# Kernel optimization log

Measured on AMD Instinct MI355X. Metric: run time of the kernel, lower is better.

Reference implementation:

```python
import jax, jax.numpy as jnp
import numpy as np

B = 4096
P = 10000          # points per cloud (hard-coded view(-1,3,10000))
NUM_POINTS = 100   # forced by phi.view(-1, 300)
BOX_SIZE = 0.5
H_G = 128
H_L = 128


def setup_inputs() -> dict:
    key = jax.random.key(0)
    ks = jax.random.split(key, 12)
    x = jax.random.uniform(ks[0], (B, 3, P, 1), dtype=jnp.float32)
    l_t_prev = jax.random.uniform(ks[1], (B, 3), dtype=jnp.float32)
    sc = 0.02
    W1 = jax.random.normal(ks[2], (H_G, NUM_POINTS * 3), dtype=jnp.float32) * sc
    b1 = jnp.zeros((H_G,), jnp.float32)
    W2 = jax.random.normal(ks[3], (H_L, 3), dtype=jnp.float32) * sc
    b2 = jnp.zeros((H_L,), jnp.float32)
    W3 = jax.random.normal(ks[4], (H_G + H_L, H_G), dtype=jnp.float32) * sc
    b3 = jnp.zeros((H_G + H_L,), jnp.float32)
    W4 = jax.random.normal(ks[5], (H_G + H_L, H_L), dtype=jnp.float32) * sc
    b4 = jnp.zeros((H_G + H_L,), jnp.float32)
    return {"x": x, "l_t_prev": l_t_prev, "W1": W1, "b1": b1, "W2": W2,
            "b2": b2, "W3": W3, "b3": b3, "W4": W4, "b4": b4}


def _foveate(x, l):
    # x: (B,3,P,1) -> pts: (B,3,P)
    pts = x.reshape(x.shape[0], 3, P)
    half = BOX_SIZE / 2.0
    lo = l - half  # (B,3)
    hi = l + half
    # per-point in-box mask over all 3 axes: (B,P)
    inside = jnp.all((pts >= lo[:, :, None]) & (pts <= hi[:, :, None]), axis=1)
    count = inside.sum(axis=-1)  # (B,)
    # stable argsort puts in-box point indices first, preserving order
    order = jnp.argsort(~inside, axis=-1, stable=True)  # (B,P)
    pos = jnp.arange(NUM_POINTS)
    # deterministic stand-in for random subsample/pad: take first NUM_POINTS
    # in-box points, wrapping (repeating) if fewer than NUM_POINTS exist
    safe = pos[None, :] % jnp.maximum(count, 1)[:, None]  # (B,NUM_POINTS)
    idx = jnp.take_along_axis(order, safe, axis=-1)  # (B,NUM_POINTS)
    idx3 = jnp.broadcast_to(idx[:, None, :], (pts.shape[0], 3, NUM_POINTS))
    sel = jnp.take_along_axis(pts, idx3, axis=2)  # (B,3,NUM_POINTS)
    # empty boxes -> zero fill (matches torch.zeros fill_box branch)
    sel = jnp.where(count[:, None, None] > 0, sel, jnp.zeros_like(sel))
    return sel.reshape(pts.shape[0], 3 * NUM_POINTS)  # (B,300)


def reference(x, l_t_prev, W1, b1, W2, b2, W3, b3, W4, b4):
    phi = _foveate(x, l_t_prev)                       # (B,300)
    phi_out = jax.nn.relu(phi @ W1.T + b1)            # (B,h_g)
    l_out = jax.nn.relu(l_t_prev @ W2.T + b2)         # (B,h_l)
    what = phi_out @ W3.T + b3                        # (B,h_g+h_l)
    where = l_out @ W4.T + b4                         # (B,h_g+h_l)
    return jax.nn.relu(what + where)
```

## Files before the change

### kernel.cpp

```cpp
#include <hip/hip_runtime.h>

#define P_PTS 10000
#define NPTS 100
#define TB 8

__global__ __launch_bounds__(256) void foveate_kernel(
    const float* __restrict__ x,
    const float* __restrict__ l,
    float* __restrict__ phi)
{
    const int b   = blockIdx.x;
    const int tid = threadIdx.x;
    const int wid = tid >> 6, lane = tid & 63;

    __shared__ float s_phi[3][NPTS];
    __shared__ int s_wcnt[4];

    const float lx = l[b * 3 + 0];
    const float ly = l[b * 3 + 1];
    const float lz = l[b * 3 + 2];
    const float lox = lx - 0.25f, hix = lx + 0.25f;
    const float loy = ly - 0.25f, hiy = ly + 0.25f;
    const float loz = lz - 0.25f, hiz = lz + 0.25f;

    const float* xb = x + (size_t)b * 3 * P_PTS;

    int cnt = 0;
    for (int base = 0; base < P_PTS; base += 256) {
        const int p = base + tid;
        bool inside = false;
        float x0 = 0.f, x1 = 0.f, x2 = 0.f;
        if (p < P_PTS) {
            x0 = xb[p];
            x1 = xb[P_PTS + p];
            x2 = xb[2 * P_PTS + p];
            inside = (x0 >= lox) && (x0 <= hix) &&
                     (x1 >= loy) && (x1 <= hiy) &&
                     (x2 >= loz) && (x2 <= hiz);
        }
        const unsigned long long m = __ballot(inside);
        if (lane == 0) s_wcnt[wid] = __popcll(m);
        __syncthreads();
        int prefix = 0, total = 0;
        #pragma unroll
        for (int w = 0; w < 4; ++w) {
            const int c = s_wcnt[w];
            total += c;
            if (w < wid) prefix += c;
        }
        const int mypos = cnt + prefix +
                          __popcll(m & ((1ull << lane) - 1ull));
        if (inside && mypos < NPTS) {
            s_phi[0][mypos] = x0;
            s_phi[1][mypos] = x1;
            s_phi[2][mypos] = x2;
        }
        cnt += total;
        __syncthreads();
        if (cnt >= NPTS) break;
    }

    const int n = (cnt < NPTS) ? cnt : NPTS;
    if (n == 0) {
        for (int j = tid; j < 3 * NPTS; j += 256)
            ((float*)s_phi)[j] = 0.0f;
    } else if (n < NPTS) {
        for (int j = n + tid; j < NPTS; j += 256) {
            const int src = j % n;
            s_phi[0][j] = s_phi[0][src];
            s_phi[1][j] = s_phi[1][src];
            s_phi[2][j] = s_phi[2][src];
        }
    }
    __syncthreads();

    for (int j = tid; j < 3 * NPTS; j += 256)
        phi[(size_t)b * 300 + j] = ((const float*)s_phi)[j];
}

__global__ __launch_bounds__(256) void mlp_kernel(
    const float* __restrict__ phi,
    const float* __restrict__ l,
    const float* __restrict__ W1,
    const float* __restrict__ b1,
    const float* __restrict__ W2,
    const float* __restrict__ b2,
    const float* __restrict__ W3,
    const float* __restrict__ b3,
    const float* __restrict__ W4,
    const float* __restrict__ b4,
    float* __restrict__ out)
{
    __shared__ float s_phi[TB][300];
    __shared__ float s_h1[TB][128];
    __shared__ float s_lo[TB][128];

    const int tid = threadIdx.x;
    const int b0  = blockIdx.x * TB;

    for (int f = tid; f < TB * 300; f += 256)
        ((float*)s_phi)[f] = phi[(size_t)b0 * 300 + f];
    __syncthreads();

    const int b  = tid >> 5;
    const int k0 = tid & 31;

    const float la = l[(b0 + b) * 3 + 0];
    const float lb = l[(b0 + b) * 3 + 1];
    const float lc = l[(b0 + b) * 3 + 2];

    float acc[4];
    #pragma unroll
    for (int j = 0; j < 4; ++j)
        acc[j] = b1[k0 + 32 * j];
    for (int i = 0; i < 300; i += 4) {
        const float4 ph = *(const float4*)&s_phi[b][i];
        #pragma unroll
        for (int j = 0; j < 4; ++j) {
            const int k = k0 + 32 * j;
            const float4 w = *(const float4*)(W1 + k * 300 + i);
            acc[j] += ph.x * w.x + ph.y * w.y + ph.z * w.z + ph.w * w.w;
        }
    }
    #pragma unroll
    for (int j = 0; j < 4; ++j) {
        const int k = k0 + 32 * j;
        s_h1[b][k] = fmaxf(acc[j], 0.0f);
        const float lo = b2[k] + la * W2[k * 3 + 0] +
                                 lb * W2[k * 3 + 1] +
                                 lc * W2[k * 3 + 2];
        s_lo[b][k] = fmaxf(lo, 0.0f);
    }
    __syncthreads();

    float acc2[8];
    #pragma unroll
    for (int j = 0; j < 8; ++j) {
        const int m = k0 + 32 * j;
        acc2[j] = b3[m] + b4[m];
    }
    for (int k = 0; k < 128; k += 4) {
        const float4 h  = *(const float4*)&s_h1[b][k];
        const float4 lo = *(const float4*)&s_lo[b][k];
        #pragma unroll
        for (int j = 0; j < 8; ++j) {
            const int m = k0 + 32 * j;
            const float4 w3 = *(const float4*)(W3 + m * 128 + k);
            const float4 w4 = *(const float4*)(W4 + m * 128 + k);
            acc2[j] += h.x  * w3.x + h.y  * w3.y + h.z  * w3.z + h.w  * w3.w +
                       lo.x * w4.x + lo.y * w4.y + lo.z * w4.z + lo.w * w4.w;
        }
    }
    #pragma unroll
    for (int j = 0; j < 8; ++j) {
        const int m = k0 + 32 * j;
        out[(size_t)(b0 + b) * 256 + m] = fmaxf(acc2[j], 0.0f);
    }
}

extern "C" void kernel_launch(void* const* d_in, const int* in_sizes, int n_in,
                              void* d_out, int out_size, void* d_ws, size_t ws_size,
                              hipStream_t stream) {
    const float* x  = (const float*)d_in[0];
    const float* l  = (const float*)d_in[1];
    const float* W1 = (const float*)d_in[2];
    const float* b1 = (const float*)d_in[3];
    const float* W2 = (const float*)d_in[4];
    const float* b2 = (const float*)d_in[5];
    const float* W3 = (const float*)d_in[6];
    const float* b3 = (const float*)d_in[7];
    const float* W4 = (const float*)d_in[8];
    const float* b4 = (const float*)d_in[9];
    float* out = (float*)d_out;
    float* phi = (float*)d_ws;

    const int B = in_sizes[1] / 3;

    foveate_kernel<<<B, 256, 0, stream>>>(x, l, phi);
    mlp_kernel<<<B / TB, 256, 0, stream>>>(phi, l, W1, b1, W2, b2,
                                           W3, b3, W4, b4, out);
}
```

Measured before the change: 745.0 us.

## Use wave-per-batch foveation with float4 prefetch and transposed-layout split MLP kernels

The foveate kernel now gives each 64-lane wave its own batch row. It reads points as float4 with a one-step register prefetch and compacts them using per-wave ballots, so the block-wide syncthreads are gone. Results are written transposed (feature-major), so the MLP is split into two kernels where each lane owns a batch column. Weights are read as wave-uniform scalars and activations as coalesced loads, and outputs are transposed back through padded shared memory. This is meant to cut per-iteration barrier overhead and uncoalesced weight traffic, at the cost of an extra launch and intermediate buffers in global memory.

```diff
diff --git a/kernel.cpp b/kernel.cpp
--- a/kernel.cpp
+++ b/kernel.cpp
@@ -1,20 +1,20 @@
 #include <hip/hip_runtime.h>
 
-#define P_PTS 10000
 #define NPTS 100
-#define TB 8
+#define P_F4 2500
 
 __global__ __launch_bounds__(256) void foveate_kernel(
     const float* __restrict__ x,
     const float* __restrict__ l,
-    float* __restrict__ phi)
+    float* __restrict__ phiT,
+    int B)
 {
-    const int b   = blockIdx.x;
-    const int tid = threadIdx.x;
-    const int wid = tid >> 6, lane = tid & 63;
+    const int tid  = threadIdx.x;
+    const int wv   = tid >> 6;
+    const int lane = tid & 63;
+    const int b    = blockIdx.x * 4 + wv;
 
-    __shared__ float s_phi[3][NPTS];
-    __shared__ int s_wcnt[4];
+    __shared__ float s_phi[4][300];
 
     const float lx = l[b * 3 + 0];
     const float ly = l[b * 3 + 1];
@@ -23,138 +23,152 @@
     const float loy = ly - 0.25f, hiy = ly + 0.25f;
     const float loz = lz - 0.25f, hiz = lz + 0.25f;
 
-    const float* xb = x + (size_t)b * 3 * P_PTS;
+    const float4* xr = (const float4*)(x + (size_t)b * 30000);
+
+    int fc = (lane < P_F4) ? lane : (P_F4 - 1);
+    float4 a = xr[fc], c = xr[P_F4 + fc], d = xr[2 * P_F4 + fc];
 
     int cnt = 0;
-    for (int base = 0; base < P_PTS; base += 256) {
-        const int p = base + tid;
-        bool inside = false;
-        float x0 = 0.f, x1 = 0.f, x2 = 0.f;
-        if (p < P_PTS) {
-            x0 = xb[p];
-            x1 = xb[P_PTS + p];
-            x2 = xb[2 * P_PTS + p];
-            inside = (x0 >= lox) && (x0 <= hix) &&
-                     (x1 >= loy) && (x1 <= hiy) &&
-                     (x2 >= loz) && (x2 <= hiz);
+    for (int base = 0; base < P_F4; base += 64) {
+        const int  f0 = base + lane;
+        const bool v  = (f0 < P_F4);
+        const float4 ca = a, cc = c, cd = d;
+        if (base + 64 < P_F4) {
+            int nf = base + 64 + lane;
+            int nfc = (nf < P_F4) ? nf : (P_F4 - 1);
+            a = xr[nfc]; c = xr[P_F4 + nfc]; d = xr[2 * P_F4 + nfc];
         }
-        const unsigned long long m = __ballot(inside);
-        if (lane == 0) s_wcnt[wid] = __popcll(m);
-        __syncthreads();
-        int prefix = 0, total = 0;
-        #pragma unroll
-        for (int w = 0; w < 4; ++w) {
-            const int c = s_wcnt[w];
-            total += c;
-            if (w < wid) prefix += c;
-        }
-        const int mypos = cnt + prefix +
-                          __popcll(m & ((1ull << lane) - 1ull));
-        if (inside && mypos < NPTS) {
-            s_phi[0][mypos] = x0;
-            s_phi[1][mypos] = x1;
-            s_phi[2][mypos] = x2;
-        }
-        cnt += total;
-        __syncthreads();
+        const bool in0 = v && ca.x >= lox && ca.x <= hix && cc.x >= loy && cc.x <= hiy && cd.x >= loz && cd.x <= hiz;
+        const bool in1 = v && ca.y >= lox && ca.y <= hix && cc.y >= loy && cc.y <= hiy && cd.y >= loz && cd.y <= hiz;
+        const bool in2 = v && ca.z >= lox && ca.z <= hix && cc.z >= loy && cc.z <= hiy && cd.z >= loz && cd.z <= hiz;
+        const bool in3 = v && ca.w >= lox && ca.w <= hix && cc.w >= loy && cc.w <= hiy && cd.w >= loz && cd.w <= hiz;
+
+        const unsigned long long m0 = __ballot(in0);
+        const unsigned long long m1 = __ballot(in1);
+        const unsigned long long m2 = __ballot(in2);
+        const unsigned long long m3 = __ballot(in3);
+        const unsigned long long below = (1ull << lane) - 1ull;
+
+        int pos = cnt + __popcll(m0 & below) + __popcll(m1 & below) +
+                        __popcll(m2 & below) + __popcll(m3 & below);
+        if (in0) { if (pos < NPTS) { s_phi[wv][pos] = ca.x; s_phi[wv][NPTS + pos] = cc.x; s_phi[wv][2 * NPTS + pos] = cd.x; } ++pos; }
+        if (in1) { if (pos < NPTS) { s_phi[wv][pos] = ca.y; s_phi[wv][NPTS + pos] = cc.y; s_phi[wv][2 * NPTS + pos] = cd.y; } ++pos; }
+        if (in2) { if (pos < NPTS) { s_phi[wv][pos] = ca.z; s_phi[wv][NPTS + pos] = cc.z; s_phi[wv][2 * NPTS + pos] = cd.z; } ++pos; }
+        if (in3) { if (pos < NPTS) { s_phi[wv][pos] = ca.w; s_phi[wv][NPTS + pos] = cc.w; s_phi[wv][2 * NPTS + pos] = cd.w; } ++pos; }
+
+        cnt += __popcll(m0) + __popcll(m1) + __popcll(m2) + __popcll(m3);
         if (cnt >= NPTS) break;
     }
 
+    __syncthreads();
+
     const int n = (cnt < NPTS) ? cnt : NPTS;
     if (n == 0) {
-        for (int j = tid; j < 3 * NPTS; j += 256)
-            ((float*)s_phi)[j] = 0.0f;
+        for (int j = lane; j < 3 * NPTS; j += 64) s_phi[wv][j] = 0.0f;
     } else if (n < NPTS) {
-        for (int j = n + tid; j < NPTS; j += 256) {
+        for (int j = n + lane; j < NPTS; j += 64) {
             const int src = j % n;
-            s_phi[0][j] = s_phi[0][src];
-            s_phi[1][j] = s_phi[1][src];
-            s_phi[2][j] = s_phi[2][src];
+            s_phi[wv][j]            = s_phi[wv][src];
+            s_phi[wv][NPTS + j]     = s_phi[wv][NPTS + src];
+            s_phi[wv][2 * NPTS + j] = s_phi[wv][2 * NPTS + src];
         }
     }
     __syncthreads();
 
-    for (int j = tid; j < 3 * NPTS; j += 256)
-        phi[(size_t)b * 300 + j] = ((const float*)s_phi)[j];
+    for (int i = lane; i < 3 * NPTS; i += 64)
+        phiT[(size_t)i * B + b] = s_phi[wv][i];
 }
 
-__global__ __launch_bounds__(256) void mlp_kernel(
-    const float* __restrict__ phi,
+__global__ __launch_bounds__(256) void mlp1_kernel(
+    const float* __restrict__ phiT,
     const float* __restrict__ l,
     const float* __restrict__ W1,
     const float* __restrict__ b1,
     const float* __restrict__ W2,
     const float* __restrict__ b2,
+    float* __restrict__ h1T,
+    float* __restrict__ loT,
+    int B)
+{
+    const int tid  = threadIdx.x;
+    const int wv   = tid >> 6;
+    const int lane = tid & 63;
+    const int BG   = B >> 6;
+    const int bg   = blockIdx.x % BG;
+    const int kh   = blockIdx.x / BG;
+    const int col  = bg * 64 + lane;
+    const int k0   = __builtin_amdgcn_readfirstlane(kh * 64 + wv * 16);
+
+    float acc[16];
+    #pragma unroll
+    for (int kk = 0; kk < 16; ++kk) acc[kk] = b1[k0 + kk];
+
+    const float* __restrict__ w1 = W1 + (size_t)k0 * 300;
+    #pragma unroll 4
+    for (int i = 0; i < 300; ++i) {
+        const float pv = phiT[(size_t)i * B + col];
+        #pragma unroll
+        for (int kk = 0; kk < 16; ++kk)
+            acc[kk] = fmaf(pv, w1[kk * 300 + i], acc[kk]);
+    }
+    #pragma unroll
+    for (int kk = 0; kk < 16; ++kk)
+        h1T[(size_t)(k0 + kk) * B + col] = fmaxf(acc[kk], 0.0f);
+
+    const float l0 = l[col * 3 + 0];
+    const float l1 = l[col * 3 + 1];
+    const float l2 = l[col * 3 + 2];
+    #pragma unroll
+    for (int kk = 0; kk < 16; ++kk) {
+        const int k = k0 + kk;
+        const float lo = b2[k] + l0 * W2[k * 3 + 0] + l1 * W2[k * 3 + 1] + l2 * W2[k * 3 + 2];
+        loT[(size_t)k * B + col] = fmaxf(lo, 0.0f);
+    }
+}
+
+__global__ __launch_bounds__(256) void mlp2_kernel(
+    const float* __restrict__ h1T,
+    const float* __restrict__ loT,
     const float* __restrict__ W3,
     const float* __restrict__ b3,
     const float* __restrict__ W4,
     const float* __restrict__ b4,
-    float* __restrict__ out)
+    float* __restrict__ out,
+    int B)
 {
-    __shared__ float s_phi[TB][300];
-    __shared__ float s_h1[TB][128];
-    __shared__ float s_lo[TB][128];
+    const int tid  = threadIdx.x;
+    const int wv   = tid >> 6;
+    const int lane = tid & 63;
+    const int BG   = B >> 6;
+    const int bg   = blockIdx.x % BG;
+    const int mq   = blockIdx.x / BG;
+    const int col  = bg * 64 + lane;
+    const int m0   = __builtin_amdgcn_readfirstlane(mq * 64 + wv * 16);
 
-    const int tid = threadIdx.x;
-    const int b0  = blockIdx.x * TB;
+    float acc[16];
+    #pragma unroll
+    for (int kk = 0; kk < 16; ++kk) acc[kk] = b3[m0 + kk] + b4[m0 + kk];
 
-    for (int f = tid; f < TB * 300; f += 256)
-        ((float*)s_phi)[f] = phi[(size_t)b0 * 300 + f];
+    const float* __restrict__ w3 = W3 + (size_t)m0 * 128;
+    const float* __restrict__ w4 = W4 + (size_t)m0 * 128;
+    #pragma unroll 2
+    for (int k = 0; k < 128; ++k) {
+        const float hv = h1T[(size_t)k * B + col];
+        const float lv = loT[(size_t)k * B + col];
+        #pragma unroll
+        for (int kk = 0; kk < 16; ++kk)
+            acc[kk] = fmaf(hv, w3[kk * 128 + k], fmaf(lv, w4[kk * 128 + k], acc[kk]));
+    }
+
+    __shared__ float s_o[64][65];
+    #pragma unroll
+    for (int kk = 0; kk < 16; ++kk)
+        s_o[wv * 16 + kk][lane] = fmaxf(acc[kk], 0.0f);
     __syncthreads();
-
-    const int b  = tid >> 5;
-    const int k0 = tid & 31;
-
-    const float la = l[(b0 + b) * 3 + 0];
-    const float lb = l[(b0 + b) * 3 + 1];
-    const float lc = l[(b0 + b) * 3 + 2];
-
-    float acc[4];
     #pragma unroll
-    for (int j = 0; j < 4; ++j)
-        acc[j] = b1[k0 + 32 * j];
-    for (int i = 0; i < 300; i += 4) {
-        const float4 ph = *(const float4*)&s_phi[b][i];
-        #pragma unroll
-        for (int j = 0; j < 4; ++j) {
-            const int k = k0 + 32 * j;
-            const float4 w = *(const float4*)(W1 + k * 300 + i);
-            acc[j] += ph.x * w.x + ph.y * w.y + ph.z * w.z + ph.w * w.w;
-        }
-    }
-    #pragma unroll
-    for (int j = 0; j < 4; ++j) {
-        const int k = k0 + 32 * j;
-        s_h1[b][k] = fmaxf(acc[j], 0.0f);
-        const float lo = b2[k] + la * W2[k * 3 + 0] +
-                                 lb * W2[k * 3 + 1] +
-                                 lc * W2[k * 3 + 2];
-        s_lo[b][k] = fmaxf(lo, 0.0f);
-    }
-    __syncthreads();
-
-    float acc2[8];
-    #pragma unroll
-    for (int j = 0; j < 8; ++j) {
-        const int m = k0 + 32 * j;
-        acc2[j] = b3[m] + b4[m];
-    }
-    for (int k = 0; k < 128; k += 4) {
-        const float4 h  = *(const float4*)&s_h1[b][k];
-        const float4 lo = *(const float4*)&s_lo[b][k];
-        #pragma unroll
-        for (int j = 0; j < 8; ++j) {
-            const int m = k0 + 32 * j;
-            const float4 w3 = *(const float4*)(W3 + m * 128 + k);
-            const float4 w4 = *(const float4*)(W4 + m * 128 + k);
-            acc2[j] += h.x  * w3.x + h.y  * w3.y + h.z  * w3.z + h.w  * w3.w +
-                       lo.x * w4.x + lo.y * w4.y + lo.z * w4.z + lo.w * w4.w;
-        }
-    }
-    #pragma unroll
-    for (int j = 0; j < 8; ++j) {
-        const int m = k0 + 32 * j;
-        out[(size_t)(b0 + b) * 256 + m] = fmaxf(acc2[j], 0.0f);
+    for (int r = 0; r < 16; ++r) {
+        const int bb = wv * 16 + r;
+        out[(size_t)(bg * 64 + bb) * 256 + mq * 64 + lane] = s_o[lane][bb];
     }
 }
 
@@ -172,11 +186,14 @@
     const float* W4 = (const float*)d_in[8];
     const float* b4 = (const float*)d_in[9];
     float* out = (float*)d_out;
-    float* phi = (float*)d_ws;
 
     const int B = in_sizes[1] / 3;
 
-    foveate_kernel<<<B, 256, 0, stream>>>(x, l, phi);
-    mlp_kernel<<<B / TB, 256, 0, stream>>>(phi, l, W1, b1, W2, b2,
-                                           W3, b3, W4, b4, out);
+    float* phiT = (float*)d_ws;
+    float* h1T  = phiT + (size_t)300 * B;
+    float* loT  = h1T  + (size_t)128 * B;
+
+    foveate_kernel<<<B / 4, 256, 0, stream>>>(x, l, phiT, B);
+    mlp1_kernel<<<2 * (B / 64), 256, 0, stream>>>(phiT, l, W1, b1, W2, b2, h1T, loT, B);
+    mlp2_kernel<<<4 * (B / 64), 256, 0, stream>>>(h1T, loT, W3, b3, W4, b4, out, B);
 }
```

New measurement: 683.6 us. 8.2% less time.
